# Kernel tuning notes

Hardware: AMD Instinct MI355X
Metric: run time of the kernel (lower is better)

The kernel has to match this reference:

```python
import jax, jax.numpy as jnp
import numpy as np

N_VARS = 8
D_MODEL = 512
L = 8192
B = 32
G = 1  # num_global_tokens
PATCH_LENS = [16, 16, 32, 32, 64, 64, 128, 128]
SAMPLING = [1, 1, 2, 2, 1, 1, 2, 2]
UNIQUE_PLS = [16, 32, 64, 128]


def _pos_emb(n, d):
    # standard sinusoidal positional embedding (Informer/Transformer style)
    pos = np.arange(n, dtype=np.float32)[:, None]
    div = np.exp(np.arange(0, d, 2, dtype=np.float32) * (-np.log(10000.0) / d))
    pe = np.zeros((n, d), dtype=np.float32)
    pe[:, 0::2] = np.sin(pos * div)
    pe[:, 1::2] = np.cos(pos * div)
    return jnp.asarray(pe)


def setup_inputs() -> dict:
    key = jax.random.key(0)
    ks = jax.random.split(key, 16)
    inp = {"x": jax.random.normal(ks[0], (B, N_VARS, L), dtype=jnp.float32)}
    # one Linear(patch_len, d_model) per unique patch_len; torch Linear weight is (out,in)
    for i, pl in enumerate(UNIQUE_PLS):
        bound = 1.0 / np.sqrt(pl)
        inp[f"w{pl}"] = jax.random.uniform(ks[1 + 2 * i], (D_MODEL, pl), minval=-bound, maxval=bound, dtype=jnp.float32)
        inp[f"b{pl}"] = jax.random.uniform(ks[2 + 2 * i], (D_MODEL,), minval=-bound, maxval=bound, dtype=jnp.float32)
    inp["glb_tokens"] = jax.random.normal(ks[10], (1, G, D_MODEL), dtype=jnp.float32)
    inp["channel_emb"] = jax.random.normal(ks[11], (N_VARS, D_MODEL), dtype=jnp.float32)
    return inp


def reference(x, w16, b16, w32, b32, w64, b64, w128, b128, glb_tokens, channel_emb):
    wdict = {16: (w16, b16), 32: (w32, b32), 64: (w64, b64), 128: (w128, b128)}
    Bn = x.shape[0]
    min_sp = min(SAMPLING)
    outs = []
    for v in range(N_VARS):
        pl = PATCH_LENS[v]
        sf = SAMPLING[v] // min_sp
        n_p = L // (pl * sf)  # num patches for this variable
        # strided gather: element j of patch i sits at i*pl*sf + j*sf -> reshape trick
        patches = x[:, v, : n_p * pl * sf].reshape(Bn, n_p, pl, sf)[..., 0]  # [B, n_p, pl]
        w, b = wdict[pl]
        emb = jnp.einsum('bnp,dp->bnd', patches, w) + b          # [B, n_p, d]
        emb = emb + _pos_emb(n_p, D_MODEL)                        # positional add
        emb = jnp.concatenate([emb, jnp.broadcast_to(glb_tokens, (Bn, G, D_MODEL))], axis=1)
        emb = emb + channel_emb[v]                                # channel add (incl. global token)
        outs.append(emb)
    return jnp.concatenate(outs, axis=1)  # [B, sum(n_p + G), d] = [32, 1608, 512]
```

## Files before the change

### kernel.cpp

```cpp
#include <hip/hip_runtime.h>
#include <math.h>

#define DM 512
#define LSEQ 8192
#define NV 8
#define TOK 1608
#define BROWS 32
#define NTHR 256

typedef _Float16 h2 __attribute__((ext_vector_type(2)));

__device__ __constant__ int c_segv[8]   = {6, 7, 4, 5, 2, 3, 0, 1};
__device__ __constant__ int c_cum[9]    = {0, 32, 64, 192, 320, 448, 576, 1088, 1600};
__device__ __constant__ int c_lgch[8]   = {0, 0, 2, 2, 2, 2, 4, 4};
__device__ __constant__ int c_tokoff[8] = {0, 513, 1026, 1155, 1284, 1413, 1542, 1575};
__device__ __constant__ int c_np[8]     = {512, 512, 128, 128, 128, 128, 32, 32};
__device__ __constant__ int c_pl[8]     = {16, 16, 32, 32, 64, 64, 128, 128};
__device__ __constant__ int c_sf[8]     = {1, 1, 2, 2, 1, 1, 2, 2};
__device__ __constant__ int c_wtoff[8]  = {262144, 262144, 266240, 266240,
                                           274432, 274432, 290816, 290816};

__device__ __forceinline__ float fdot2f(h2 a, h2 b, float c) {
#if __has_builtin(__builtin_amdgcn_fdot2)
    return __builtin_amdgcn_fdot2(a, b, c, false);
#else
    return fmaf((float)a.y, (float)b.y, fmaf((float)a.x, (float)b.x, c));
#endif
}
__device__ __forceinline__ h2 bch2(unsigned u) { return __builtin_bit_cast(h2, u); }

__global__ __launch_bounds__(512) void setup_kernel(
    const float* __restrict__ w16, const float* __restrict__ w32,
    const float* __restrict__ w64, const float* __restrict__ w128,
    float* __restrict__ ws)
{
    int bid = blockIdx.x;
    int d = threadIdx.x;
    if (bid < 512) {
        int idx = bid * 512 + d;
        int i = idx >> 9;
        int dd = idx & (DM - 1);
        const float c = -9.210340371976184f / 512.0f;
        float div = expf((float)(dd & ~1) * c);
        float ang = (float)i * div;
        ws[idx] = (dd & 1) ? cosf(ang) : sinf(ang);
        return;
    }
    int j = bid - 512;
    const float* w; int pl, k2, off;
    if (j < 8)       { w = w16;  pl = 16;  k2 = j;      off = 262144; }
    else if (j < 24) { w = w32;  pl = 32;  k2 = j - 8;  off = 266240; }
    else if (j < 56) { w = w64;  pl = 64;  k2 = j - 24; off = 274432; }
    else             { w = w128; pl = 128; k2 = j - 56; off = 290816; }
    float2 p = *reinterpret_cast<const float2*>(w + (size_t)d * pl + 2 * k2);
    h2 h; h.x = (_Float16)p.x; h.y = (_Float16)p.y;
    reinterpret_cast<unsigned*>(ws)[off + k2 * DM + d] = __builtin_bit_cast(unsigned, h);
}

__global__ __launch_bounds__(NTHR) void patch_embed_kernel(
    const float* __restrict__ x,
    const float* __restrict__ b16,  const float* __restrict__ b32,
    const float* __restrict__ b64,  const float* __restrict__ b128,
    const float* __restrict__ glb,  const float* __restrict__ chan,
    const float* __restrict__ ws,   float* __restrict__ out)
{
    extern __shared__ float ldsf[];
    unsigned* ldsu = reinterpret_cast<unsigned*>(ldsf);
    int bid = blockIdx.x;
    const int tid = threadIdx.x;

    if (bid >= 1600) {
        int v = bid - 1600;
        int d2 = tid << 1;
        float2 g = *reinterpret_cast<const float2*>(glb + d2);
        float2 c = *reinterpret_cast<const float2*>(chan + v * DM + d2);
        float2 o; o.x = g.x + c.x; o.y = g.y + c.y;
        int row0 = c_tokoff[v] + c_np[v];
        for (int b = 0; b < 32; ++b)
            *reinterpret_cast<float2*>(out + ((size_t)(b * TOK + row0)) * DM + d2) = o;
        return;
    }

    int seg = 0;
    while (bid >= c_cum[seg + 1]) ++seg;
    int local = bid - c_cum[seg];
    int v = c_segv[seg];
    int lg = c_lgch[seg];
    int b = local >> lg;
    int chunk = local & ((1 << lg) - 1);
    const int pl = c_pl[v];
    const int sf = c_sf[v];
    const int pl2 = pl >> 1;
    const int i0 = chunk * BROWS;

    const int ne2 = (BROWS * pl) >> 1;
    const float* xb = x + ((size_t)b * NV + v) * LSEQ + (size_t)i0 * (pl * sf);
    if (sf == 1) {
        for (int t = tid; t < (ne2 >> 1); t += NTHR) {
            float4 q = *reinterpret_cast<const float4*>(xb + 4 * t);
            h2 a; a.x = (_Float16)q.x; a.y = (_Float16)q.y;
            h2 c; c.x = (_Float16)q.z; c.y = (_Float16)q.w;
            uint2 o; o.x = __builtin_bit_cast(unsigned, a);
            o.y = __builtin_bit_cast(unsigned, c);
            *reinterpret_cast<uint2*>(ldsu + 2 * t) = o;
        }
    } else {
        for (int p = tid; p < ne2; p += NTHR) {
            float4 q = *reinterpret_cast<const float4*>(xb + 4 * p);
            h2 a; a.x = (_Float16)q.x; a.y = (_Float16)q.z;
            ldsu[p] = __builtin_bit_cast(unsigned, a);
        }
    }
    __syncthreads();

    const int lane = tid & 63;
    const int wv   = tid >> 6;
    const int c0   = lane << 3;
    const unsigned* prow = ldsu + (wv * 8) * pl2;
    const unsigned* wtv  = reinterpret_cast<const unsigned*>(ws) + c_wtoff[v];

    float acc[8][8];
#pragma unroll
    for (int r = 0; r < 8; ++r)
#pragma unroll
        for (int c = 0; c < 8; ++c) acc[r][c] = 0.f;

    uint4 wa0 = *reinterpret_cast<const uint4*>(wtv + c0);
    uint4 wb0 = *reinterpret_cast<const uint4*>(wtv + c0 + 4);
    uint4 wa1 = *reinterpret_cast<const uint4*>(wtv + DM + c0);
    uint4 wb1 = *reinterpret_cast<const uint4*>(wtv + DM + c0 + 4);

    for (int k2 = 0; k2 < pl2; k2 += 2) {
        uint4 na0, nb0, na1, nb1;
        if (k2 + 2 < pl2) {
            const unsigned* wn = wtv + (k2 + 2) * DM;
            na0 = *reinterpret_cast<const uint4*>(wn + c0);
            nb0 = *reinterpret_cast<const uint4*>(wn + c0 + 4);
            na1 = *reinterpret_cast<const uint4*>(wn + DM + c0);
            nb1 = *reinterpret_cast<const uint4*>(wn + DM + c0 + 4);
        }
        uint2 pr[8];
#pragma unroll
        for (int r = 0; r < 8; ++r)
            pr[r] = *reinterpret_cast<const uint2*>(prow + r * pl2 + k2);
#pragma unroll
        for (int r = 0; r < 8; ++r) {
            h2 p0 = bch2(pr[r].x);
            h2 p1 = bch2(pr[r].y);
            acc[r][0] = fdot2f(p1, bch2(wa1.x), fdot2f(p0, bch2(wa0.x), acc[r][0]));
            acc[r][1] = fdot2f(p1, bch2(wa1.y), fdot2f(p0, bch2(wa0.y), acc[r][1]));
            acc[r][2] = fdot2f(p1, bch2(wa1.z), fdot2f(p0, bch2(wa0.z), acc[r][2]));
            acc[r][3] = fdot2f(p1, bch2(wa1.w), fdot2f(p0, bch2(wa0.w), acc[r][3]));
            acc[r][4] = fdot2f(p1, bch2(wb1.x), fdot2f(p0, bch2(wb0.x), acc[r][4]));
            acc[r][5] = fdot2f(p1, bch2(wb1.y), fdot2f(p0, bch2(wb0.y), acc[r][5]));
            acc[r][6] = fdot2f(p1, bch2(wb1.z), fdot2f(p0, bch2(wb0.z), acc[r][6]));
            acc[r][7] = fdot2f(p1, bch2(wb1.w), fdot2f(p0, bch2(wb0.w), acc[r][7]));
        }
        wa0 = na0; wb0 = nb0; wa1 = na1; wb1 = nb1;
    }

    const float* bias = (pl == 16) ? b16 : (pl == 32) ? b32 : (pl == 64) ? b64 : b128;
    float4 bcA, bcB;
    {
        float4 ba = *reinterpret_cast<const float4*>(bias + c0);
        float4 bb = *reinterpret_cast<const float4*>(bias + c0 + 4);
        float4 ca = *reinterpret_cast<const float4*>(chan + v * DM + c0);
        float4 cb = *reinterpret_cast<const float4*>(chan + v * DM + c0 + 4);
        bcA.x = ba.x + ca.x; bcA.y = ba.y + ca.y; bcA.z = ba.z + ca.z; bcA.w = ba.w + ca.w;
        bcB.x = bb.x + cb.x; bcB.y = bb.y + cb.y; bcB.z = bb.z + cb.z; bcB.w = bb.w + cb.w;
    }

    const int row0 = i0 + wv * 8;
    float* ob = out + ((size_t)(b * TOK + c_tokoff[v] + row0)) * DM + c0;
    const float* pb = ws  + (size_t)row0 * DM + c0;
#pragma unroll
    for (int r = 0; r < 8; ++r) {
        float4 pA = *reinterpret_cast<const float4*>(pb + (size_t)r * DM);
        float4 pB = *reinterpret_cast<const float4*>(pb + (size_t)r * DM + 4);
        float4 oA, oB;
        oA.x = acc[r][0] + bcA.x + pA.x;
        oA.y = acc[r][1] + bcA.y + pA.y;
        oA.z = acc[r][2] + bcA.z + pA.z;
        oA.w = acc[r][3] + bcA.w + pA.w;
        oB.x = acc[r][4] + bcB.x + pB.x;
        oB.y = acc[r][5] + bcB.y + pB.y;
        oB.z = acc[r][6] + bcB.z + pB.z;
        oB.w = acc[r][7] + bcB.w + pB.w;
        *reinterpret_cast<float4*>(ob + (size_t)r * DM)     = oA;
        *reinterpret_cast<float4*>(ob + (size_t)r * DM + 4) = oB;
    }
}

extern "C" void kernel_launch(void* const* d_in, const int* in_sizes, int n_in,
                              void* d_out, int out_size, void* d_ws, size_t ws_size,
                              hipStream_t stream) {
    const float* x    = (const float*)d_in[0];
    const float* w16  = (const float*)d_in[1];
    const float* b16  = (const float*)d_in[2];
    const float* w32  = (const float*)d_in[3];
    const float* b32  = (const float*)d_in[4];
    const float* w64  = (const float*)d_in[5];
    const float* b64  = (const float*)d_in[6];
    const float* w128 = (const float*)d_in[7];
    const float* b128 = (const float*)d_in[8];
    const float* glb  = (const float*)d_in[9];
    const float* chan = (const float*)d_in[10];
    float* out = (float*)d_out;
    float* ws  = (float*)d_ws;

    hipLaunchKernelGGL(setup_kernel, dim3(632), dim3(512), 0, stream,
                       w16, w32, w64, w128, ws);
    hipLaunchKernelGGL(patch_embed_kernel, dim3(1608), dim3(NTHR),
                       BROWS * 64 * sizeof(unsigned),
                       stream,
                       x, b16, b32, b64, b128, glb, chan, ws, out);
}
```

Baseline: 42.84 us.

## Template patch kernel on patch length, widen LDS reads, use nontemporal stores

The patch embedding body becomes a template specialised on patch length and sampling factor, so the K loop is fully unrolled with compile-time bounds. The inner loop now reads 8 fp16 pairs per row with 128-bit LDS loads and prefetches 8 weight vectors per step. Output stores become nontemporal, and launch bounds ask for 3 blocks per CU. Together these aim to cut loop overhead, LDS traffic and cache pollution from the large output write. The cost is higher register pressure and larger code from the unrolled template instances.

Result: slower. 86.25 us (+101.3%).

```diff
diff --git a/kernel.cpp b/kernel.cpp
--- a/kernel.cpp
+++ b/kernel.cpp
@@ -9,14 +9,13 @@
 #define NTHR 256
 
 typedef _Float16 h2 __attribute__((ext_vector_type(2)));
+typedef float f4n __attribute__((ext_vector_type(4)));
 
 __device__ __constant__ int c_segv[8]   = {6, 7, 4, 5, 2, 3, 0, 1};
 __device__ __constant__ int c_cum[9]    = {0, 32, 64, 192, 320, 448, 576, 1088, 1600};
 __device__ __constant__ int c_lgch[8]   = {0, 0, 2, 2, 2, 2, 4, 4};
 __device__ __constant__ int c_tokoff[8] = {0, 513, 1026, 1155, 1284, 1413, 1542, 1575};
 __device__ __constant__ int c_np[8]     = {512, 512, 128, 128, 128, 128, 32, 32};
-__device__ __constant__ int c_pl[8]     = {16, 16, 32, 32, 64, 64, 128, 128};
-__device__ __constant__ int c_sf[8]     = {1, 1, 2, 2, 1, 1, 2, 2};
 __device__ __constant__ int c_wtoff[8]  = {262144, 262144, 266240, 266240,
                                            274432, 274432, 290816, 290816};
 
@@ -28,6 +27,15 @@
 #endif
 }
 __device__ __forceinline__ h2 bch2(unsigned u) { return __builtin_bit_cast(h2, u); }
+
+__device__ __forceinline__ void nt_store4(float* p, float4 v) {
+#if __has_builtin(__builtin_nontemporal_store)
+    f4n t; t.x = v.x; t.y = v.y; t.z = v.z; t.w = v.w;
+    __builtin_nontemporal_store(t, reinterpret_cast<f4n*>(p));
+#else
+    *reinterpret_cast<float4*>(p) = v;
+#endif
+}
 
 __global__ __launch_bounds__(512) void setup_kernel(
     const float* __restrict__ w16, const float* __restrict__ w32,
@@ -57,46 +65,22 @@
     reinterpret_cast<unsigned*>(ws)[off + k2 * DM + d] = __builtin_bit_cast(unsigned, h);
 }
 
-__global__ __launch_bounds__(NTHR) void patch_embed_kernel(
-    const float* __restrict__ x,
-    const float* __restrict__ b16,  const float* __restrict__ b32,
-    const float* __restrict__ b64,  const float* __restrict__ b128,
-    const float* __restrict__ glb,  const float* __restrict__ chan,
-    const float* __restrict__ ws,   float* __restrict__ out)
+template<int PL, int SF>
+__device__ __forceinline__ void patch_block(
+    const float* __restrict__ x, unsigned* __restrict__ ldsu,
+    const float* __restrict__ bias, const float* __restrict__ chan,
+    const float* __restrict__ ws, float* __restrict__ out,
+    int v, int b, int i0, int tokoff)
 {
-    extern __shared__ float ldsf[];
-    unsigned* ldsu = reinterpret_cast<unsigned*>(ldsf);
-    int bid = blockIdx.x;
+    constexpr int PL2 = PL >> 1;
+    constexpr int NK8 = PL >> 3;
     const int tid = threadIdx.x;
 
-    if (bid >= 1600) {
-        int v = bid - 1600;
-        int d2 = tid << 1;
-        float2 g = *reinterpret_cast<const float2*>(glb + d2);
-        float2 c = *reinterpret_cast<const float2*>(chan + v * DM + d2);
-        float2 o; o.x = g.x + c.x; o.y = g.y + c.y;
-        int row0 = c_tokoff[v] + c_np[v];
-        for (int b = 0; b < 32; ++b)
-            *reinterpret_cast<float2*>(out + ((size_t)(b * TOK + row0)) * DM + d2) = o;
-        return;
-    }
-
-    int seg = 0;
-    while (bid >= c_cum[seg + 1]) ++seg;
-    int local = bid - c_cum[seg];
-    int v = c_segv[seg];
-    int lg = c_lgch[seg];
-    int b = local >> lg;
-    int chunk = local & ((1 << lg) - 1);
-    const int pl = c_pl[v];
-    const int sf = c_sf[v];
-    const int pl2 = pl >> 1;
-    const int i0 = chunk * BROWS;
-
-    const int ne2 = (BROWS * pl) >> 1;
-    const float* xb = x + ((size_t)b * NV + v) * LSEQ + (size_t)i0 * (pl * sf);
-    if (sf == 1) {
-        for (int t = tid; t < (ne2 >> 1); t += NTHR) {
+    constexpr int NE2 = (BROWS * PL) >> 1;
+    const float* xb = x + ((size_t)b * NV + v) * LSEQ + (size_t)i0 * (PL * SF);
+    if (SF == 1) {
+#pragma unroll
+        for (int t = tid; t < (NE2 >> 1); t += NTHR) {
             float4 q = *reinterpret_cast<const float4*>(xb + 4 * t);
             h2 a; a.x = (_Float16)q.x; a.y = (_Float16)q.y;
             h2 c; c.x = (_Float16)q.z; c.y = (_Float16)q.w;
@@ -105,7 +89,8 @@
             *reinterpret_cast<uint2*>(ldsu + 2 * t) = o;
         }
     } else {
-        for (int p = tid; p < ne2; p += NTHR) {
+#pragma unroll
+        for (int p = tid; p < NE2; p += NTHR) {
             float4 q = *reinterpret_cast<const float4*>(xb + 4 * p);
             h2 a; a.x = (_Float16)q.x; a.y = (_Float16)q.z;
             ldsu[p] = __builtin_bit_cast(unsigned, a);
@@ -116,7 +101,7 @@
     const int lane = tid & 63;
     const int wv   = tid >> 6;
     const int c0   = lane << 3;
-    const unsigned* prow = ldsu + (wv * 8) * pl2;
+    const unsigned* prow = ldsu + (wv * 8) * PL2;
     const unsigned* wtv  = reinterpret_cast<const unsigned*>(ws) + c_wtoff[v];
 
     float acc[8][8];
@@ -125,41 +110,53 @@
 #pragma unroll
         for (int c = 0; c < 8; ++c) acc[r][c] = 0.f;
 
-    uint4 wa0 = *reinterpret_cast<const uint4*>(wtv + c0);
-    uint4 wb0 = *reinterpret_cast<const uint4*>(wtv + c0 + 4);
-    uint4 wa1 = *reinterpret_cast<const uint4*>(wtv + DM + c0);
-    uint4 wb1 = *reinterpret_cast<const uint4*>(wtv + DM + c0 + 4);
-
-    for (int k2 = 0; k2 < pl2; k2 += 2) {
-        uint4 na0, nb0, na1, nb1;
-        if (k2 + 2 < pl2) {
-            const unsigned* wn = wtv + (k2 + 2) * DM;
-            na0 = *reinterpret_cast<const uint4*>(wn + c0);
-            nb0 = *reinterpret_cast<const uint4*>(wn + c0 + 4);
-            na1 = *reinterpret_cast<const uint4*>(wn + DM + c0);
-            nb1 = *reinterpret_cast<const uint4*>(wn + DM + c0 + 4);
-        }
-        uint2 pr[8];
-#pragma unroll
-        for (int r = 0; r < 8; ++r)
-            pr[r] = *reinterpret_cast<const uint2*>(prow + r * pl2 + k2);
-#pragma unroll
-        for (int r = 0; r < 8; ++r) {
-            h2 p0 = bch2(pr[r].x);
-            h2 p1 = bch2(pr[r].y);
-            acc[r][0] = fdot2f(p1, bch2(wa1.x), fdot2f(p0, bch2(wa0.x), acc[r][0]));
-            acc[r][1] = fdot2f(p1, bch2(wa1.y), fdot2f(p0, bch2(wa0.y), acc[r][1]));
-            acc[r][2] = fdot2f(p1, bch2(wa1.z), fdot2f(p0, bch2(wa0.z), acc[r][2]));
-            acc[r][3] = fdot2f(p1, bch2(wa1.w), fdot2f(p0, bch2(wa0.w), acc[r][3]));
-            acc[r][4] = fdot2f(p1, bch2(wb1.x), fdot2f(p0, bch2(wb0.x), acc[r][4]));
-            acc[r][5] = fdot2f(p1, bch2(wb1.y), fdot2f(p0, bch2(wb0.y), acc[r][5]));
-            acc[r][6] = fdot2f(p1, bch2(wb1.z), fdot2f(p0, bch2(wb0.z), acc[r][6]));
-            acc[r][7] = fdot2f(p1, bch2(wb1.w), fdot2f(p0, bch2(wb0.w), acc[r][7]));
-        }
-        wa0 = na0; wb0 = nb0; wa1 = na1; wb1 = nb1;
-    }
-
-    const float* bias = (pl == 16) ? b16 : (pl == 32) ? b32 : (pl == 64) ? b64 : b128;
+    uint4 wc[8], wn[8];
+#pragma unroll
+    for (int j = 0; j < 8; ++j)
+        wc[j] = *reinterpret_cast<const uint4*>(wtv + (j >> 1) * DM + c0 + (j & 1) * 4);
+
+#pragma unroll
+    for (int k8 = 0; k8 < NK8; ++k8) {
+        if (k8 + 1 < NK8) {
+            const unsigned* wnp = wtv + (size_t)(k8 + 1) * 4 * DM;
+#pragma unroll
+            for (int j = 0; j < 8; ++j)
+                wn[j] = *reinterpret_cast<const uint4*>(wnp + (j >> 1) * DM + c0 + (j & 1) * 4);
+        }
+#pragma unroll
+        for (int rp = 0; rp < 4; ++rp) {
+            uint4 pa = *reinterpret_cast<const uint4*>(prow + (2 * rp)     * PL2 + k8 * 4);
+            uint4 pb = *reinterpret_cast<const uint4*>(prow + (2 * rp + 1) * PL2 + k8 * 4);
+#pragma unroll
+            for (int t = 0; t < 4; ++t) {
+                unsigned ua = (t == 0) ? pa.x : (t == 1) ? pa.y : (t == 2) ? pa.z : pa.w;
+                unsigned ub = (t == 0) ? pb.x : (t == 1) ? pb.y : (t == 2) ? pb.z : pb.w;
+                h2 qa = bch2(ua), qb = bch2(ub);
+                uint4 wA = wc[2 * t], wB = wc[2 * t + 1];
+                acc[2*rp][0] = fdot2f(qa, bch2(wA.x), acc[2*rp][0]);
+                acc[2*rp][1] = fdot2f(qa, bch2(wA.y), acc[2*rp][1]);
+                acc[2*rp][2] = fdot2f(qa, bch2(wA.z), acc[2*rp][2]);
+                acc[2*rp][3] = fdot2f(qa, bch2(wA.w), acc[2*rp][3]);
+                acc[2*rp][4] = fdot2f(qa, bch2(wB.x), acc[2*rp][4]);
+                acc[2*rp][5] = fdot2f(qa, bch2(wB.y), acc[2*rp][5]);
+                acc[2*rp][6] = fdot2f(qa, bch2(wB.z), acc[2*rp][6]);
+                acc[2*rp][7] = fdot2f(qa, bch2(wB.w), acc[2*rp][7]);
+                acc[2*rp+1][0] = fdot2f(qb, bch2(wA.x), acc[2*rp+1][0]);
+                acc[2*rp+1][1] = fdot2f(qb, bch2(wA.y), acc[2*rp+1][1]);
+                acc[2*rp+1][2] = fdot2f(qb, bch2(wA.z), acc[2*rp+1][2]);
+                acc[2*rp+1][3] = fdot2f(qb, bch2(wA.w), acc[2*rp+1][3]);
+                acc[2*rp+1][4] = fdot2f(qb, bch2(wB.x), acc[2*rp+1][4]);
+                acc[2*rp+1][5] = fdot2f(qb, bch2(wB.y), acc[2*rp+1][5]);
+                acc[2*rp+1][6] = fdot2f(qb, bch2(wB.z), acc[2*rp+1][6]);
+                acc[2*rp+1][7] = fdot2f(qb, bch2(wB.w), acc[2*rp+1][7]);
+            }
+        }
+        if (k8 + 1 < NK8) {
+#pragma unroll
+            for (int j = 0; j < 8; ++j) wc[j] = wn[j];
+        }
+    }
+
     float4 bcA, bcB;
     {
         float4 ba = *reinterpret_cast<const float4*>(bias + c0);
@@ -171,7 +168,7 @@
     }
 
     const int row0 = i0 + wv * 8;
-    float* ob = out + ((size_t)(b * TOK + c_tokoff[v] + row0)) * DM + c0;
+    float* ob = out + ((size_t)(b * TOK + tokoff + row0)) * DM + c0;
     const float* pb = ws  + (size_t)row0 * DM + c0;
 #pragma unroll
     for (int r = 0; r < 8; ++r) {
@@ -186,8 +183,54 @@
         oB.y = acc[r][5] + bcB.y + pB.y;
         oB.z = acc[r][6] + bcB.z + pB.z;
         oB.w = acc[r][7] + bcB.w + pB.w;
-        *reinterpret_cast<float4*>(ob + (size_t)r * DM)     = oA;
-        *reinterpret_cast<float4*>(ob + (size_t)r * DM + 4) = oB;
+        nt_store4(ob + (size_t)r * DM,     oA);
+        nt_store4(ob + (size_t)r * DM + 4, oB);
+    }
+}
+
+__global__ __launch_bounds__(NTHR, 3) void patch_embed_kernel(
+    const float* __restrict__ x,
+    const float* __restrict__ b16,  const float* __restrict__ b32,
+    const float* __restrict__ b64,  const float* __restrict__ b128,
+    const float* __restrict__ glb,  const float* __restrict__ chan,
+    const float* __restrict__ ws,   float* __restrict__ out)
+{
+    extern __shared__ float ldsf[];
+    unsigned* ldsu = reinterpret_cast<unsigned*>(ldsf);
+    int bid = blockIdx.x;
+    const int tid = threadIdx.x;
+
+    if (bid >= 1600) {
+        int v = bid - 1600;
+        int d2 = tid << 1;
+        float2 g = *reinterpret_cast<const float2*>(glb + d2);
+        float2 c = *reinterpret_cast<const float2*>(chan + v * DM + d2);
+        float2 o; o.x = g.x + c.x; o.y = g.y + c.y;
+        int row0 = c_tokoff[v] + c_np[v];
+        for (int b = 0; b < 32; ++b)
+            *reinterpret_cast<float2*>(out + ((size_t)(b * TOK + row0)) * DM + d2) = o;
+        return;
+    }
+
+    int seg = 0;
+    while (bid >= c_cum[seg + 1]) ++seg;
+    int local = bid - c_cum[seg];
+    int v = c_segv[seg];
+    int lg = c_lgch[seg];
+    int b = local >> lg;
+    int chunk = local & ((1 << lg) - 1);
+    int i0 = chunk * BROWS;
+    int tokoff = c_tokoff[v];
+
+    switch (v) {
+        case 0: patch_block<16, 1>(x, ldsu, b16,  chan, ws, out, 0, b, i0, tokoff); break;
+        case 1: patch_block<16, 1>(x, ldsu, b16,  chan, ws, out, 1, b, i0, tokoff); break;
+        case 2: patch_block<32, 2>(x, ldsu, b32,  chan, ws, out, 2, b, i0, tokoff); break;
+        case 3: patch_block<32, 2>(x, ldsu, b32,  chan, ws, out, 3, b, i0, tokoff); break;
+        case 4: patch_block<64, 1>(x, ldsu, b64,  chan, ws, out, 4, b, i0, tokoff); break;
+        case 5: patch_block<64, 1>(x, ldsu, b64,  chan, ws, out, 5, b, i0, tokoff); break;
+        case 6: patch_block<128,2>(x, ldsu, b128, chan, ws, out, 6, b, i0, tokoff); break;
+        case 7: patch_block<128,2>(x, ldsu, b128, chan, ws, out, 7, b, i0, tokoff); break;
     }
 }
 
```
